# Kernel tuning notes

Measured on AMD Instinct MI355X. Metric: run time of the kernel, lower is better.

Reference implementation:

```python
import jax, jax.numpy as jnp
import numpy as np

T_STEPS = 4
LAYERS = 10
CYCLE = 10
C = 64
TAU = 1.2
V_TH = 0.5
SG_ALPHA = 4.0  # spikingjelly default surrogate.Sigmoid alpha


@jax.custom_vjp
def heaviside_sg(x):
    return (x >= 0.0).astype(x.dtype)

def _h_fwd(x):
    return heaviside_sg(x), x

def _h_bwd(x, g):
    s = jax.nn.sigmoid(SG_ALPHA * x)
    return (SG_ALPHA * s * (1.0 - s) * g,)

heaviside_sg.defvjp(_h_fwd, _h_bwd)


def lif(x_seq):
    # MultiStepLIFNode: v' = v + (x - (v - v_reset))/tau, hard reset to v_reset=0,
    # detach_reset=True -> spike in reset path is stop-gradient'ed.
    def step(v, x):
        v = v + (x - v) / TAU
        spike = heaviside_sg(v - V_TH)
        v = v * (1.0 - jax.lax.stop_gradient(spike))
        return v, spike
    _, spikes = jax.lax.scan(step, jnp.zeros_like(x_seq[0]), x_seq)
    return spikes


def conv_seq(x, w, b, dilation=1):
    # x: [T,B,Cin,L]; w: [Cout,Cin,K]; 'same' padding for odd K
    T, B, Ci, L = x.shape
    K = w.shape[-1]
    pad = (K - 1) * dilation // 2
    y = jax.lax.conv_general_dilated(
        x.reshape(T * B, Ci, L), w, (1,), [(pad, pad)],
        rhs_dilation=(dilation,), dimension_numbers=('NCH', 'OIH', 'NCH'))
    y = y + b[None, :, None]
    return y.reshape(T, B, -1, L)


def setup_inputs() -> dict:
    key = jax.random.key(0)
    ks = jax.random.split(key, 20)
    B, L = 4, 4096
    s = 0.1
    n = jax.random.normal
    inp = {
        'audio': jax.random.uniform(ks[0], (B, L), dtype=jnp.float32),
        'diffusion_step': jax.random.randint(ks[1], (B,), 0, 50),
        'W_in': n(ks[2], (C, 1, 1), jnp.float32) * s,
        'b_in': n(ks[3], (C,), jnp.float32) * s,
        'demb_w1': n(ks[4], (LAYERS, C, 1), jnp.float32) * s,
        'demb_b1': n(ks[5], (LAYERS, C), jnp.float32) * s,
        'demb_w2': n(ks[6], (LAYERS, C, C), jnp.float32) * s,
        'demb_b2': n(ks[7], (LAYERS, C), jnp.float32) * s,
        'dproj_w': n(ks[8], (LAYERS, C, C), jnp.float32) * s,
        'dproj_b': n(ks[9], (LAYERS, C), jnp.float32) * s,
        'conv_w': n(ks[10], (LAYERS, 2 * C, C, 3), jnp.float32) * 0.05,
        'conv_b': n(ks[11], (LAYERS, 2 * C), jnp.float32) * s,
        'skip_w': n(ks[12], (LAYERS, C, C, 1), jnp.float32) * s,
        'skip_b': n(ks[13], (LAYERS, C), jnp.float32) * s,
        'res_w': n(ks[14], (LAYERS, C, C, 1), jnp.float32) * s,
        'res_b': n(ks[15], (LAYERS, C), jnp.float32) * s,
        'W_out': n(ks[16], (1, C, 1), jnp.float32) * s,
        'b_out': n(ks[17], (1,), jnp.float32) * s,
    }
    return inp


def reference(audio, diffusion_step, W_in, b_in, demb_w1, demb_b1, demb_w2,
              demb_b2, dproj_w, dproj_b, conv_w, conv_b, skip_w, skip_b,
              res_w, res_b, W_out, b_out):
    B, L = audio.shape
    # Poisson encoder: spike = 1[u < x] per timestep (fixed key -> deterministic)
    u = jax.random.uniform(jax.random.key(42), (T_STEPS, B, 1, L), dtype=jnp.float32)
    spike_seq = (u < audio[None, :, None, :]).astype(jnp.float32)

    x = conv_seq(spike_seq, W_in, b_in)          # [T,B,C,L]
    x = lif(x)

    d = diffusion_step.astype(jnp.float32)[:, None]  # [B,1]
    total_skip = jnp.zeros_like(x)
    for i in range(LAYERS):
        dilation = 2 ** (i % CYCLE)
        emb = jax.nn.silu(d @ demb_w1[i].T + demb_b1[i]) @ demb_w2[i].T + demb_b2[i]  # [B,C]
        proj = emb @ dproj_w[i].T + dproj_b[i]                                        # [B,C]
        y = x + proj[None, :, :, None]
        y = conv_seq(y, conv_w[i], conv_b[i], dilation=dilation)  # [T,B,2C,L]
        y = lif(y)
        gate, filt = jnp.split(y, 2, axis=2)
        y = jax.nn.sigmoid(gate) * jnp.tanh(filt)
        total_skip = total_skip + conv_seq(y, skip_w[i], skip_b[i])
        x = x + conv_seq(y, res_w[i], res_b[i])

    total_skip = jax.nn.relu(total_skip)
    out = conv_seq(total_skip, W_out, b_out)  # [T,B,1,L]
    out = lif(out)
    return out.sum(axis=0)  # [B,1,L]
```

## Files before the change

### kernel.cpp

```cpp
#include <hip/hip_runtime.h>

#define LL 4096
#define NB 4
#define NC 64
#define NT 4
#define NLAYERS 10
#define XS 5120
#define XPAD 512

__device__ __forceinline__ void threefry2x32(unsigned x0, unsigned x1,
                                             unsigned& o0, unsigned& o1) {
  const unsigned ks0 = 0u, ks1 = 42u;
  const unsigned ks2 = 0x1BD11BDAu ^ ks0 ^ ks1;
  const unsigned ks[3] = {ks0, ks1, ks2};
  const unsigned r0[4] = {13u, 15u, 26u, 6u};
  const unsigned r1[4] = {17u, 29u, 16u, 24u};
  x0 += ks0; x1 += ks1;
#pragma unroll
  for (int g = 0; g < 5; ++g) {
    const unsigned* rr = (g & 1) ? r1 : r0;
#pragma unroll
    for (int j = 0; j < 4; ++j) {
      x0 += x1;
      unsigned r = rr[j];
      x1 = (x1 << r) | (x1 >> (32u - r));
      x1 ^= x0;
    }
    x0 += ks[(g + 1) % 3];
    x1 += ks[(g + 2) % 3] + (unsigned)(g + 1);
  }
  o0 = x0; o1 = x1;
}

__device__ __forceinline__ float u01(unsigned bits) {
  return __uint_as_float((bits >> 9) | 0x3f800000u) - 1.0f;
}

__device__ __forceinline__ float lif_step(float& v, float xt) {
  v = v + (xt - v) / 1.2f;
  float s = (v >= 0.5f) ? 1.0f : 0.0f;
  v = v * (1.0f - s);
  return s;
}

__global__ void prep_kernel(const float* __restrict__ skip_w,
                            const float* __restrict__ res_w,
                            const float* __restrict__ conv_w,
                            float* __restrict__ skipT,
                            float* __restrict__ resT,
                            float* __restrict__ wT) {
  int i = blockIdx.x;
  for (int idx = threadIdx.x; idx < 4096; idx += 256) {
    int c = idx >> 6, cp = idx & 63;
    skipT[i * 4096 + cp * 64 + c] = skip_w[i * 4096 + c * 64 + cp];
    resT[i * 4096 + cp * 64 + c] = res_w[i * 4096 + c * 64 + cp];
  }
  for (int idx = threadIdx.x; idx < 8 * 64 * 3 * 16; idx += 256) {
    int col = idx & 15;
    int r = idx >> 4;
    int k = r % 3; r /= 3;
    int ci = r % 64;
    int g = r / 64;
    int co = (col < 8) ? (g * 8 + col) : (64 + g * 8 + (col - 8));
    wT[i * 24576 + idx] = conv_w[(i * 128 + co) * 192 + ci * 3 + k];
  }
}

__global__ void proj_kernel(const int* __restrict__ dstep,
                            const float* __restrict__ w1, const float* __restrict__ b1,
                            const float* __restrict__ w2, const float* __restrict__ b2,
                            const float* __restrict__ pw, const float* __restrict__ pb,
                            float* __restrict__ proj) {
  __shared__ float e1[NB][NC];
  __shared__ float e2[NB][NC];
  int i = blockIdx.x;
  int tid = threadIdx.x;
  int b = tid >> 6, c = tid & 63;
  float d = (float)dstep[b];
  float v = d * w1[i * 64 + c] + b1[i * 64 + c];
  v = v / (1.0f + expf(-v));
  e1[b][c] = v;
  __syncthreads();
  float a = b2[i * 64 + c];
  for (int cp = 0; cp < 64; ++cp) a += e1[b][cp] * w2[(i * 64 + c) * 64 + cp];
  e2[b][c] = a;
  __syncthreads();
  float p = pb[i * 64 + c];
  for (int cp = 0; cp < 64; ++cp) p += e2[b][cp] * pw[(i * 64 + c) * 64 + cp];
  proj[(i * 4 + b) * 64 + c] = p;
}

__global__ void pc_kernel(const float* __restrict__ proj,
                          const float* __restrict__ conv_w,
                          float* __restrict__ pc) {
  __shared__ float pv[64];
  int layer = blockIdx.x, b = blockIdx.y;
  int tid = threadIdx.x;
  if (tid < 64) pv[tid] = proj[(layer * 4 + b) * 64 + tid];
  __syncthreads();
  int co = tid;
  const float* w = conv_w + (layer * 128 + co) * 192;
  float s0 = 0.0f, s1 = 0.0f, s2 = 0.0f;
  for (int ci = 0; ci < 64; ++ci) {
    float p = pv[ci];
    s0 += p * w[ci * 3 + 0];
    s1 += p * w[ci * 3 + 1];
    s2 += p * w[ci * 3 + 2];
  }
  float* o = pc + ((layer * 4 + b) * 128 + co) * 3;
  o[0] = s0; o[1] = s1; o[2] = s2;
}

__global__ void padzero_kernel(float* __restrict__ x) {
  int row = blockIdx.x;
  float* base = x + (size_t)row * XS;
  for (int i = threadIdx.x; i < XPAD; i += 256) {
    base[i] = 0.0f;
    base[XPAD + LL + i] = 0.0f;
  }
}

__global__ void encode_lif_kernel(const float* __restrict__ audio,
                                  const float* __restrict__ W_in,
                                  const float* __restrict__ b_in,
                                  float* __restrict__ x) {
  int tid = threadIdx.x;
  int lq = tid & 63, grp = tid >> 6;
  int l = blockIdx.x * 64 + lq;
  int b = blockIdx.y;
  float a = audio[b * LL + l];
  unsigned p0 = (unsigned)(b * LL + l);
  unsigned p1 = 16384u + p0;
  unsigned o00, o01, o10, o11;
  threefry2x32(p0, p0 + 32768u, o00, o01);
  threefry2x32(p1, p1 + 32768u, o10, o11);
  float sp[4];
  sp[0] = (u01(o00) < a) ? 1.0f : 0.0f;
  sp[1] = (u01(o10) < a) ? 1.0f : 0.0f;
  sp[2] = (u01(o01) < a) ? 1.0f : 0.0f;
  sp[3] = (u01(o11) < a) ? 1.0f : 0.0f;
  for (int j = 0; j < 16; ++j) {
    int c = grp * 16 + j;
    float w = W_in[c], bb = b_in[c];
    float v = 0.0f;
#pragma unroll
    for (int t = 0; t < 4; ++t) {
      float s = lif_step(v, w * sp[t] + bb);
      x[(size_t)((t * 4 + b) * 64 + c) * XS + XPAD + l] = s;
    }
  }
}

template <int DIL>
__global__ __launch_bounds__(256) void layer_conv_kernel(
    const float* __restrict__ x, const float* __restrict__ wT,
    const float* __restrict__ conv_b, const float* __restrict__ pc,
    float* __restrict__ y, int layer) {
  __shared__ float wg_lds[192 * 8];
  int tid = threadIdx.x;
  int g = blockIdx.y;
  int b = blockIdx.z;
  int l = blockIdx.x * 256 + tid;
  const float* wbase = wT + (size_t)(layer * 8 + g) * 3072;

  for (int idx = tid; idx < 1536; idx += 256) {
    wg_lds[idx] = wbase[(idx >> 3) * 16 + (idx & 7)];
  }
  __syncthreads();

  const float* px[4];
#pragma unroll
  for (int t = 0; t < 4; ++t)
    px[t] = x + (size_t)((t * 4 + b) * 64) * XS + XPAD + l;

  float ag[32], af[32];
#pragma unroll
  for (int q = 0; q < 32; ++q) { ag[q] = 0.0f; af[q] = 0.0f; }

  float xa[12], xb[12];
  auto loadx = [&](float* dst) {
#pragma unroll
    for (int t = 0; t < 4; ++t) {
      dst[t * 3 + 0] = px[t][-DIL];
      dst[t * 3 + 1] = px[t][0];
      dst[t * 3 + 2] = px[t][DIL];
      px[t] += XS;
    }
  };
  auto compute = [&](int ci, const float* xv) {
#pragma unroll
    for (int k = 0; k < 3; ++k) {
      const float4 g0 = *(const float4*)&wg_lds[(ci * 3 + k) * 8];
      const float4 g1 = *(const float4*)&wg_lds[(ci * 3 + k) * 8 + 4];
      const float4 f0 = *(const float4*)&wbase[(ci * 3 + k) * 16 + 8];
      const float4 f1 = *(const float4*)&wbase[(ci * 3 + k) * 16 + 12];
#pragma unroll
      for (int t = 0; t < 4; ++t) {
        float xq = xv[t * 3 + k];
        ag[t * 8 + 0] += g0.x * xq; ag[t * 8 + 1] += g0.y * xq;
        ag[t * 8 + 2] += g0.z * xq; ag[t * 8 + 3] += g0.w * xq;
        ag[t * 8 + 4] += g1.x * xq; ag[t * 8 + 5] += g1.y * xq;
        ag[t * 8 + 6] += g1.z * xq; ag[t * 8 + 7] += g1.w * xq;
        af[t * 8 + 0] += f0.x * xq; af[t * 8 + 1] += f0.y * xq;
        af[t * 8 + 2] += f0.z * xq; af[t * 8 + 3] += f0.w * xq;
        af[t * 8 + 4] += f1.x * xq; af[t * 8 + 5] += f1.y * xq;
        af[t * 8 + 6] += f1.z * xq; af[t * 8 + 7] += f1.w * xq;
      }
    }
  };

  loadx(xa);
  for (int ci = 0; ci < 64; ci += 2) {
    loadx(xb);
    compute(ci, xa);
    if (ci + 2 < 64) loadx(xa);
    compute(ci + 1, xb);
  }

  const float SIG1 = 0.73105857863000489f;
  const float TANH1 = 0.76159415595576486f;
  bool lb = (l < DIL), rb = (l >= LL - DIL);
#pragma unroll
  for (int j = 0; j < 8; ++j) {
    int cog = g * 8 + j;
    int cof = 64 + g * 8 + j;
    const float* pg = pc + ((layer * 4 + b) * 128 + cog) * 3;
    const float* pf = pc + ((layer * 4 + b) * 128 + cof) * 3;
    float S0g = pg[0], S1g = pg[1], S2g = pg[2];
    float S0f = pf[0], S1f = pf[1], S2f = pf[2];
    float bg = conv_b[layer * 128 + cog] + S0g + S1g + S2g;
    float bf = conv_b[layer * 128 + cof] + S0f + S1f + S2f;
    bg -= (lb ? S0g : 0.0f) + (rb ? S2g : 0.0f);
    bf -= (lb ? S0f : 0.0f) + (rb ? S2f : 0.0f);
    float vg = 0.0f, vf = 0.0f;
#pragma unroll
    for (int t = 0; t < 4; ++t) {
      float sg = lif_step(vg, ag[t * 8 + j] + bg);
      float sf = lif_step(vf, af[t * 8 + j] + bf);
      float gv = (sg != 0.0f) ? SIG1 : 0.5f;
      float tv = (sf != 0.0f) ? TANH1 : 0.0f;
      y[(size_t)((t * 4 + b) * 64 + cog) * LL + l] = gv * tv;
    }
  }
}

__global__ __launch_bounds__(256) void skip_res_kernel(
    const float* __restrict__ y, const float* __restrict__ skipT,
    const float* __restrict__ resT, const float* __restrict__ skip_b,
    const float* __restrict__ res_b, float* __restrict__ tskip,
    float* __restrict__ x, int layer) {
  int tid = threadIdx.x;
  int lg = tid & 31;
  int cg = tid >> 5;
  int cv = blockIdx.y;
  int tb = blockIdx.z;
  int l0 = blockIdx.x * 256 + lg * 8;
  int c0 = cg * 8;

  const float* wsrc = (cv ? resT : skipT) + layer * 4096 + c0;
  const float* yb = y + (size_t)tb * 64 * LL + l0;

  float acc[64];
#pragma unroll
  for (int q = 0; q < 64; ++q) acc[q] = 0.0f;

  float4 w0a = *(const float4*)&wsrc[0];
  float4 w1a = *(const float4*)&wsrc[4];
  float4 y0a = *(const float4*)&yb[0];
  float4 y1a = *(const float4*)&yb[4];

  for (int cp = 0; cp < 64; ++cp) {
    int cpn = (cp < 63) ? cp + 1 : 63;
    float4 w0b = *(const float4*)&wsrc[cpn * 64];
    float4 w1b = *(const float4*)&wsrc[cpn * 64 + 4];
    float4 y0b = *(const float4*)&yb[(size_t)cpn * LL];
    float4 y1b = *(const float4*)&yb[(size_t)cpn * LL + 4];

    float wv[8] = {w0a.x, w0a.y, w0a.z, w0a.w, w1a.x, w1a.y, w1a.z, w1a.w};
    float yv[8] = {y0a.x, y0a.y, y0a.z, y0a.w, y1a.x, y1a.y, y1a.z, y1a.w};
#pragma unroll
    for (int i = 0; i < 8; ++i)
#pragma unroll
      for (int j = 0; j < 8; ++j) acc[i * 8 + j] += wv[i] * yv[j];

    w0a = w0b; w1a = w1b; y0a = y0b; y1a = y1b;
  }

  const float* bsrc = (cv ? res_b : skip_b) + layer * 64 + c0;
#pragma unroll
  for (int i = 0; i < 8; ++i) {
    float bb = bsrc[i];
    if (cv == 0) {
      size_t idx = (size_t)(tb * 64 + c0 + i) * LL + l0;
      float4 o0, o1;
      if (layer == 0) {
        o0.x = o0.y = o0.z = o0.w = 0.0f;
        o1 = o0;
      } else {
        o0 = *(const float4*)&tskip[idx];
        o1 = *(const float4*)&tskip[idx + 4];
      }
      o0.x += acc[i * 8 + 0] + bb; o0.y += acc[i * 8 + 1] + bb;
      o0.z += acc[i * 8 + 2] + bb; o0.w += acc[i * 8 + 3] + bb;
      o1.x += acc[i * 8 + 4] + bb; o1.y += acc[i * 8 + 5] + bb;
      o1.z += acc[i * 8 + 6] + bb; o1.w += acc[i * 8 + 7] + bb;
      *(float4*)&tskip[idx] = o0;
      *(float4*)&tskip[idx + 4] = o1;
    } else {
      size_t idx = (size_t)(tb * 64 + c0 + i) * XS + XPAD + l0;
      float4 o0 = *(const float4*)&x[idx];
      float4 o1 = *(const float4*)&x[idx + 4];
      o0.x += acc[i * 8 + 0] + bb; o0.y += acc[i * 8 + 1] + bb;
      o0.z += acc[i * 8 + 2] + bb; o0.w += acc[i * 8 + 3] + bb;
      o1.x += acc[i * 8 + 4] + bb; o1.y += acc[i * 8 + 5] + bb;
      o1.z += acc[i * 8 + 6] + bb; o1.w += acc[i * 8 + 7] + bb;
      *(float4*)&x[idx] = o0;
      *(float4*)&x[idx + 4] = o1;
    }
  }
}

__global__ void out_kernel(const float* __restrict__ tskip,
                           const float* __restrict__ W_out,
                           const float* __restrict__ b_out,
                           float* __restrict__ out) {
  __shared__ float red[4][4][64];
  int tid = threadIdx.x;
  int lq = tid & 63, grp = tid >> 6;
  int l = blockIdx.x * 64 + lq;
  int b = blockIdx.y;
  float acc[4] = {0.0f, 0.0f, 0.0f, 0.0f};
  for (int j = 0; j < 16; ++j) {
    int c = grp * 16 + j;
    float w = W_out[c];
#pragma unroll
    for (int t = 0; t < 4; ++t) {
      float sv = tskip[(size_t)((t * 4 + b) * 64 + c) * LL + l];
      acc[t] += fmaxf(sv, 0.0f) * w;
    }
  }
#pragma unroll
  for (int t = 0; t < 4; ++t) red[grp][t][lq] = acc[t];
  __syncthreads();
  if (grp == 0) {
    float bo = b_out[0];
    float v = 0.0f, s = 0.0f;
#pragma unroll
    for (int t = 0; t < 4; ++t) {
      float a = red[0][t][lq] + red[1][t][lq] + red[2][t][lq] + red[3][t][lq] + bo;
      s += lif_step(v, a);
    }
    out[b * LL + l] = s;
  }
}

extern "C" void kernel_launch(void* const* d_in, const int* in_sizes, int n_in,
                              void* d_out, int out_size, void* d_ws, size_t ws_size,
                              hipStream_t stream) {
  const float* audio   = (const float*)d_in[0];
  const int*   dstep   = (const int*)d_in[1];
  const float* W_in    = (const float*)d_in[2];
  const float* b_in    = (const float*)d_in[3];
  const float* demb_w1 = (const float*)d_in[4];
  const float* demb_b1 = (const float*)d_in[5];
  const float* demb_w2 = (const float*)d_in[6];
  const float* demb_b2 = (const float*)d_in[7];
  const float* dproj_w = (const float*)d_in[8];
  const float* dproj_b = (const float*)d_in[9];
  const float* conv_w  = (const float*)d_in[10];
  const float* conv_b  = (const float*)d_in[11];
  const float* skip_w  = (const float*)d_in[12];
  const float* skip_b  = (const float*)d_in[13];
  const float* res_w   = (const float*)d_in[14];
  const float* res_b   = (const float*)d_in[15];
  const float* W_out   = (const float*)d_in[16];
  const float* b_out   = (const float*)d_in[17];
  float* out = (float*)d_out;
  float* ws = (float*)d_ws;

  float* proj  = ws;
  float* skipT = proj + 2560;
  float* resT  = skipT + 40960;
  float* pc    = resT + 40960;
  float* wT    = pc + 15360;
  float* x     = wT + 245760;
  float* y     = x + 5242880;
  float* tskip = y + 4194304;

  prep_kernel<<<10, 256, 0, stream>>>(skip_w, res_w, conv_w, skipT, resT, wT);
  proj_kernel<<<10, 256, 0, stream>>>(dstep, demb_w1, demb_b1, demb_w2, demb_b2,
                                      dproj_w, dproj_b, proj);
  pc_kernel<<<dim3(10, 4), 128, 0, stream>>>(proj, conv_w, pc);
  padzero_kernel<<<1024, 256, 0, stream>>>(x);
  encode_lif_kernel<<<dim3(64, 4), 256, 0, stream>>>(audio, W_in, b_in, x);

  for (int i = 0; i < NLAYERS; ++i) {
    dim3 gc(16, 8, 4);
    switch (i) {
      case 0: layer_conv_kernel<1><<<gc, 256, 0, stream>>>(x, wT, conv_b, pc, y, i); break;
      case 1: layer_conv_kernel<2><<<gc, 256, 0, stream>>>(x, wT, conv_b, pc, y, i); break;
      case 2: layer_conv_kernel<4><<<gc, 256, 0, stream>>>(x, wT, conv_b, pc, y, i); break;
      case 3: layer_conv_kernel<8><<<gc, 256, 0, stream>>>(x, wT, conv_b, pc, y, i); break;
      case 4: layer_conv_kernel<16><<<gc, 256, 0, stream>>>(x, wT, conv_b, pc, y, i); break;
      case 5: layer_conv_kernel<32><<<gc, 256, 0, stream>>>(x, wT, conv_b, pc, y, i); break;
      case 6: layer_conv_kernel<64><<<gc, 256, 0, stream>>>(x, wT, conv_b, pc, y, i); break;
      case 7: layer_conv_kernel<128><<<gc, 256, 0, stream>>>(x, wT, conv_b, pc, y, i); break;
      case 8: layer_conv_kernel<256><<<gc, 256, 0, stream>>>(x, wT, conv_b, pc, y, i); break;
      case 9: layer_conv_kernel<512><<<gc, 256, 0, stream>>>(x, wT, conv_b, pc, y, i); break;
    }
    skip_res_kernel<<<dim3(16, 2, 16), 256, 0, stream>>>(y, skipT, resT, skip_b,
                                                         res_b, tskip, x, i);
  }
  out_kernel<<<dim3(64, 4), 256, 0, stream>>>(tskip, W_out, b_out, out);
}
```

Before: 910.2 us.

## Split conv input channels across half-blocks and shrink skip/res tiles for more blocks

```diff
diff --git a/kernel.cpp b/kernel.cpp
--- a/kernel.cpp
+++ b/kernel.cpp
@@ -157,10 +157,12 @@
     const float* __restrict__ conv_b, const float* __restrict__ pc,
     float* __restrict__ y, int layer) {
   __shared__ float wg_lds[192 * 8];
-  int tid = threadIdx.x;
+  __shared__ float comb[128 * 33];
+  int tid = threadIdx.x;
+  int lt = tid & 127, h = tid >> 7;
   int g = blockIdx.y;
   int b = blockIdx.z;
-  int l = blockIdx.x * 256 + tid;
+  int l = blockIdx.x * 128 + lt;
   const float* wbase = wT + (size_t)(layer * 8 + g) * 3072;
 
   for (int idx = tid; idx < 1536; idx += 256) {
@@ -171,7 +173,7 @@
   const float* px[4];
 #pragma unroll
   for (int t = 0; t < 4; ++t)
-    px[t] = x + (size_t)((t * 4 + b) * 64) * XS + XPAD + l;
+    px[t] = x + (size_t)((t * 4 + b) * 64 + h * 32) * XS + XPAD + l;
 
   float ag[32], af[32];
 #pragma unroll
@@ -209,37 +211,58 @@
     }
   };
 
+  int cib = h * 32;
   loadx(xa);
-  for (int ci = 0; ci < 64; ci += 2) {
+  for (int cl = 0; cl < 32; cl += 2) {
     loadx(xb);
-    compute(ci, xa);
-    if (ci + 2 < 64) loadx(xa);
-    compute(ci + 1, xb);
-  }
-
-  const float SIG1 = 0.73105857863000489f;
-  const float TANH1 = 0.76159415595576486f;
-  bool lb = (l < DIL), rb = (l >= LL - DIL);
-#pragma unroll
-  for (int j = 0; j < 8; ++j) {
-    int cog = g * 8 + j;
-    int cof = 64 + g * 8 + j;
-    const float* pg = pc + ((layer * 4 + b) * 128 + cog) * 3;
-    const float* pf = pc + ((layer * 4 + b) * 128 + cof) * 3;
-    float S0g = pg[0], S1g = pg[1], S2g = pg[2];
-    float S0f = pf[0], S1f = pf[1], S2f = pf[2];
-    float bg = conv_b[layer * 128 + cog] + S0g + S1g + S2g;
-    float bf = conv_b[layer * 128 + cof] + S0f + S1f + S2f;
-    bg -= (lb ? S0g : 0.0f) + (rb ? S2g : 0.0f);
-    bf -= (lb ? S0f : 0.0f) + (rb ? S2f : 0.0f);
-    float vg = 0.0f, vf = 0.0f;
-#pragma unroll
-    for (int t = 0; t < 4; ++t) {
-      float sg = lif_step(vg, ag[t * 8 + j] + bg);
-      float sf = lif_step(vf, af[t * 8 + j] + bf);
-      float gv = (sg != 0.0f) ? SIG1 : 0.5f;
-      float tv = (sf != 0.0f) ? TANH1 : 0.0f;
-      y[(size_t)((t * 4 + b) * 64 + cog) * LL + l] = gv * tv;
+    compute(cib + cl, xa);
+    if (cl + 2 < 32) loadx(xa);
+    compute(cib + cl + 1, xb);
+  }
+
+  if (h == 1) {
+#pragma unroll
+    for (int q = 0; q < 32; ++q) comb[lt * 33 + q] = ag[q];
+  }
+  __syncthreads();
+  if (h == 0) {
+#pragma unroll
+    for (int q = 0; q < 32; ++q) ag[q] += comb[lt * 33 + q];
+  }
+  __syncthreads();
+  if (h == 1) {
+#pragma unroll
+    for (int q = 0; q < 32; ++q) comb[lt * 33 + q] = af[q];
+  }
+  __syncthreads();
+  if (h == 0) {
+#pragma unroll
+    for (int q = 0; q < 32; ++q) af[q] += comb[lt * 33 + q];
+
+    const float SIG1 = 0.73105857863000489f;
+    const float TANH1 = 0.76159415595576486f;
+    bool lb = (l < DIL), rb = (l >= LL - DIL);
+#pragma unroll
+    for (int j = 0; j < 8; ++j) {
+      int cog = g * 8 + j;
+      int cof = 64 + g * 8 + j;
+      const float* pg = pc + ((layer * 4 + b) * 128 + cog) * 3;
+      const float* pf = pc + ((layer * 4 + b) * 128 + cof) * 3;
+      float S0g = pg[0], S1g = pg[1], S2g = pg[2];
+      float S0f = pf[0], S1f = pf[1], S2f = pf[2];
+      float bg = conv_b[layer * 128 + cog] + S0g + S1g + S2g;
+      float bf = conv_b[layer * 128 + cof] + S0f + S1f + S2f;
+      bg -= (lb ? S0g : 0.0f) + (rb ? S2g : 0.0f);
+      bf -= (lb ? S0f : 0.0f) + (rb ? S2f : 0.0f);
+      float vg = 0.0f, vf = 0.0f;
+#pragma unroll
+      for (int t = 0; t < 4; ++t) {
+        float sg = lif_step(vg, ag[t * 8 + j] + bg);
+        float sf = lif_step(vf, af[t * 8 + j] + bf);
+        float gv = (sg != 0.0f) ? SIG1 : 0.5f;
+        float tv = (sf != 0.0f) ? TANH1 : 0.0f;
+        y[(size_t)((t * 4 + b) * 64 + cog) * LL + l] = gv * tv;
+      }
     }
   }
 }
@@ -254,36 +277,35 @@
   int cg = tid >> 5;
   int cv = blockIdx.y;
   int tb = blockIdx.z;
-  int l0 = blockIdx.x * 256 + lg * 8;
+  int l0 = blockIdx.x * 128 + lg * 4;
   int c0 = cg * 8;
 
   const float* wsrc = (cv ? resT : skipT) + layer * 4096 + c0;
   const float* yb = y + (size_t)tb * 64 * LL + l0;
 
-  float acc[64];
-#pragma unroll
-  for (int q = 0; q < 64; ++q) acc[q] = 0.0f;
+  float acc[32];
+#pragma unroll
+  for (int q = 0; q < 32; ++q) acc[q] = 0.0f;
 
   float4 w0a = *(const float4*)&wsrc[0];
   float4 w1a = *(const float4*)&wsrc[4];
   float4 y0a = *(const float4*)&yb[0];
-  float4 y1a = *(const float4*)&yb[4];
 
   for (int cp = 0; cp < 64; ++cp) {
     int cpn = (cp < 63) ? cp + 1 : 63;
     float4 w0b = *(const float4*)&wsrc[cpn * 64];
     float4 w1b = *(const float4*)&wsrc[cpn * 64 + 4];
     float4 y0b = *(const float4*)&yb[(size_t)cpn * LL];
-    float4 y1b = *(const float4*)&yb[(size_t)cpn * LL + 4];
 
     float wv[8] = {w0a.x, w0a.y, w0a.z, w0a.w, w1a.x, w1a.y, w1a.z, w1a.w};
-    float yv[8] = {y0a.x, y0a.y, y0a.z, y0a.w, y1a.x, y1a.y, y1a.z, y1a.w};
-#pragma unroll
-    for (int i = 0; i < 8; ++i)
-#pragma unroll
-      for (int j = 0; j < 8; ++j) acc[i * 8 + j] += wv[i] * yv[j];
-
-    w0a = w0b; w1a = w1b; y0a = y0b; y1a = y1b;
+#pragma unroll
+    for (int i = 0; i < 8; ++i) {
+      acc[i * 4 + 0] += wv[i] * y0a.x;
+      acc[i * 4 + 1] += wv[i] * y0a.y;
+      acc[i * 4 + 2] += wv[i] * y0a.z;
+      acc[i * 4 + 3] += wv[i] * y0a.w;
+    }
+    w0a = w0b; w1a = w1b; y0a = y0b;
   }
 
   const float* bsrc = (cv ? res_b : skip_b) + layer * 64 + c0;
@@ -292,30 +314,21 @@
     float bb = bsrc[i];
     if (cv == 0) {
       size_t idx = (size_t)(tb * 64 + c0 + i) * LL + l0;
-      float4 o0, o1;
+      float4 o0;
       if (layer == 0) {
         o0.x = o0.y = o0.z = o0.w = 0.0f;
-        o1 = o0;
       } else {
         o0 = *(const float4*)&tskip[idx];
-        o1 = *(const float4*)&tskip[idx + 4];
       }
-      o0.x += acc[i * 8 + 0] + bb; o0.y += acc[i * 8 + 1] + bb;
-      o0.z += acc[i * 8 + 2] + bb; o0.w += acc[i * 8 + 3] + bb;
-      o1.x += acc[i * 8 + 4] + bb; o1.y += acc[i * 8 + 5] + bb;
-      o1.z += acc[i * 8 + 6] + bb; o1.w += acc[i * 8 + 7] + bb;
+      o0.x += acc[i * 4 + 0] + bb; o0.y += acc[i * 4 + 1] + bb;
+      o0.z += acc[i * 4 + 2] + bb; o0.w += acc[i * 4 + 3] + bb;
       *(float4*)&tskip[idx] = o0;
-      *(float4*)&tskip[idx + 4] = o1;
     } else {
       size_t idx = (size_t)(tb * 64 + c0 + i) * XS + XPAD + l0;
       float4 o0 = *(const float4*)&x[idx];
-      float4 o1 = *(const float4*)&x[idx + 4];
-      o0.x += acc[i * 8 + 0] + bb; o0.y += acc[i * 8 + 1] + bb;
-      o0.z += acc[i * 8 + 2] + bb; o0.w += acc[i * 8 + 3] + bb;
-      o1.x += acc[i * 8 + 4] + bb; o1.y += acc[i * 8 + 5] + bb;
-      o1.z += acc[i * 8 + 6] + bb; o1.w += acc[i * 8 + 7] + bb;
+      o0.x += acc[i * 4 + 0] + bb; o0.y += acc[i * 4 + 1] + bb;
+      o0.z += acc[i * 4 + 2] + bb; o0.w += acc[i * 4 + 3] + bb;
       *(float4*)&x[idx] = o0;
-      *(float4*)&x[idx + 4] = o1;
     }
   }
 }
@@ -395,7 +408,7 @@
   encode_lif_kernel<<<dim3(64, 4), 256, 0, stream>>>(audio, W_in, b_in, x);
 
   for (int i = 0; i < NLAYERS; ++i) {
-    dim3 gc(16, 8, 4);
+    dim3 gc(32, 8, 4);
     switch (i) {
       case 0: layer_conv_kernel<1><<<gc, 256, 0, stream>>>(x, wT, conv_b, pc, y, i); break;
       case 1: layer_conv_kernel<2><<<gc, 256, 0, stream>>>(x, wT, conv_b, pc, y, i); break;
@@ -408,7 +421,7 @@
       case 8: layer_conv_kernel<256><<<gc, 256, 0, stream>>>(x, wT, conv_b, pc, y, i); break;
       case 9: layer_conv_kernel<512><<<gc, 256, 0, stream>>>(x, wT, conv_b, pc, y, i); break;
     }
-    skip_res_kernel<<<dim3(16, 2, 16), 256, 0, stream>>>(y, skipT, resT, skip_b,
+    skip_res_kernel<<<dim3(32, 2, 16), 256, 0, stream>>>(y, skipT, resT, skip_b,
                                                          res_b, tskip, x, i);
   }
   out_kernel<<<dim3(64, 4), 256, 0, stream>>>(tskip, W_out, b_out, out);
```

Result: slower. 1.065 ms (+17.0%).
